# Optimization experiments

Measured on AMD Instinct MI355X. Metric: run time of the kernel, lower is better.

The kernel has to match this reference:

```python
import jax, jax.numpy as jnp
import numpy as np

N_QUBITS = 6
N_LAYERS = 2
QSVT_DEGREE = 3
DT_RANK = max(N_QUBITS // 2, 1)
OUT_DIM = 3 * N_QUBITS
PI = np.float32(np.pi)
DT_MIN, DT_MAX = 1e-3, 0.1
BATCH, SEQ = 256, 512


def _ry_mat(theta):
    c = jnp.cos(theta / 2)
    s = jnp.sin(theta / 2)
    row0 = jnp.stack([c, -s], axis=-1)
    row1 = jnp.stack([s, c], axis=-1)
    return jnp.stack([row0, row1], axis=-2).astype(jnp.complex64)


def _rz_mat(theta):
    e = jnp.exp(-0.5j * theta.astype(jnp.complex64))
    z = jnp.zeros_like(e)
    row0 = jnp.stack([e, z], axis=-1)
    row1 = jnp.stack([z, jnp.conj(e)], axis=-1)
    return jnp.stack([row0, row1], axis=-2)


def _rx_mat(theta):
    c = jnp.cos(theta / 2).astype(jnp.complex64)
    s = jnp.sin(theta / 2).astype(jnp.complex64)
    row0 = jnp.stack([c, -1j * s], axis=-1)
    row1 = jnp.stack([-1j * s, c], axis=-1)
    return jnp.stack([row0, row1], axis=-2)


def _apply1(state, mat, w):
    # state: (B, 2, ..., 2) tensor over N_QUBITS axes; mat: (2,2) or batched (B,2,2)
    state = jnp.moveaxis(state, 1 + w, -1)
    if mat.ndim == 3:
        state = jnp.einsum('bij,b...j->b...i', mat, state)
    else:
        state = jnp.einsum('ij,b...j->b...i', mat, state)
    return jnp.moveaxis(state, -1, 1 + w)


def _cnot(state, c, t):
    state = jnp.moveaxis(state, (1 + c, 1 + t), (-2, -1))
    state = state.at[..., 1, :].set(state[..., 1, ::-1])
    return jnp.moveaxis(state, (-2, -1), (1 + c, 1 + t))


def _crx(state, theta, c, t):
    state = jnp.moveaxis(state, (1 + c, 1 + t), (-2, -1))
    m = _rx_mat(theta)
    state = state.at[..., 1, :].set(jnp.einsum('ij,...j->...i', m, state[..., 1, :]))
    return jnp.moveaxis(state, (-2, -1), (1 + c, 1 + t))


def _circuit(h, x, dt, circuit_params, poly_coeffs, qsvt_params):
    """Batched statevector simulation of the selective QSVT + unified ansatz qnode."""
    n = N_QUBITS
    B = h.shape[0]
    state = jnp.zeros((B,) + (2,) * n, jnp.complex64)
    state = state.at[(slice(None),) + (0,) * n].set(1.0 + 0.0j)
    # 1) state encoding RY(h[t-1])
    for i in range(n):
        state = _apply1(state, _ry_mat(h[:, i]), i)
    # 2) Delta-modulated QSVT: RZ rotations + bidirectional CNOT ring per degree
    qidx = 0
    n_qp = n * QSVT_DEGREE
    for deg in range(QSVT_DEGREE + 1):
        coeff = poly_coeffs[deg]
        for i in range(n):
            if qidx < n_qp:
                ang = coeff * dt[:, i] * qsvt_params[qidx] * PI
                qidx += 1
            else:
                ang = coeff * dt[:, i] * PI
            state = _apply1(state, _rz_mat(ang), i)
        for i in range(n - 1):
            state = _cnot(state, i, i + 1)
        state = _cnot(state, n - 1, 0)
        for i in range(n - 1, 0, -1):
            state = _cnot(state, i, i - 1)
    # 3) unified variational ansatz
    p = 0
    for _ in range(N_LAYERS):
        for i in range(n):
            state = _apply1(state, _rx_mat(circuit_params[p]), i)
            state = _apply1(state, _ry_mat(circuit_params[p + 1]), i)
            state = _apply1(state, _rz_mat(circuit_params[p + 2]), i)
            p += 3
        for i in range(n):
            state = _crx(state, circuit_params[p], i, (i + 1) % n)
            p += 1
        for i in range(n - 1, -1, -1):
            state = _crx(state, circuit_params[p], i, (i - 1) % n)
            p += 1
    # 4) Delta-modulated input RY(x * dt)
    for i in range(n):
        state = _apply1(state, _ry_mat(x[:, i] * dt[:, i]), i)
    # 5) Pauli X/Y/Z expectation values per qubit
    xs, ys, zs = [], [], []
    for i in range(n):
        s = jnp.moveaxis(state, 1 + i, 1).reshape(B, 2, -1)
        z = jnp.sum(jnp.conj(s[:, 0]) * s[:, 1], axis=-1)
        xs.append(2.0 * jnp.real(z))
        ys.append(2.0 * jnp.imag(z))
        zs.append(jnp.sum(jnp.abs(s[:, 0]) ** 2 - jnp.abs(s[:, 1]) ** 2, axis=-1))
    return jnp.stack(xs + ys + zs, axis=-1).astype(jnp.float32)  # (B, 3n)


def setup_inputs() -> dict:
    key = jax.random.key(0)
    ks = jax.random.split(key, 8)
    angles = jax.random.uniform(ks[0], (BATCH, SEQ, N_QUBITS), jnp.float32) * PI
    Wx = jax.random.normal(ks[1], (DT_RANK + 2 * N_QUBITS, N_QUBITS), jnp.float32) / np.float32(np.sqrt(N_QUBITS))
    Wdt = jax.random.normal(ks[2], (N_QUBITS, DT_RANK), jnp.float32) / np.float32(np.sqrt(DT_RANK))
    dt = jnp.exp(jax.random.uniform(ks[3], (N_QUBITS,), jnp.float32) * np.float32(np.log(DT_MAX) - np.log(DT_MIN)) + np.float32(np.log(DT_MIN)))
    bdt = dt + jnp.log(-jnp.expm1(-dt))
    poly_coeffs = jax.random.normal(ks[4], (QSVT_DEGREE + 1,), jnp.float32) * 0.1
    qsvt_params = jax.random.normal(ks[5], (N_QUBITS * QSVT_DEGREE,), jnp.float32) * 0.1
    circuit_params = jax.random.normal(ks[6], (5 * N_QUBITS * N_LAYERS,), jnp.float32) * 0.1
    D = jnp.ones((OUT_DIM,), jnp.float32)
    Wc = jax.random.normal(ks[7], (OUT_DIM, N_QUBITS), jnp.float32) / np.float32(np.sqrt(N_QUBITS))
    return {"angles": angles, "Wx": Wx, "Wdt": Wdt, "bdt": bdt, "poly_coeffs": poly_coeffs, "qsvt_params": qsvt_params, "circuit_params": circuit_params, "D": D, "Wc": Wc}


def reference(angles, Wx, Wdt, bdt, poly_coeffs, qsvt_params, circuit_params, D, Wc):
    x_dbc = angles @ Wx.T  # (B,S, dt_rank + 2n)
    dt_raw = x_dbc[..., :DT_RANK]
    # B slice computed in the original but never used in forward
    C = x_dbc[..., DT_RANK + N_QUBITS:]
    dt_angles = jnp.tanh(jax.nn.softplus(dt_raw @ Wdt.T + bdt)) * PI  # (B,S,n)
    # quantum part is detached in the original (detach().cpu() before the qnode)
    sg = jax.lax.stop_gradient
    xs = (jnp.moveaxis(sg(angles), 1, 0), jnp.moveaxis(sg(dt_angles), 1, 0))
    cp, pc, qp = sg(circuit_params), sg(poly_coeffs), sg(qsvt_params)
    h0 = jnp.zeros((angles.shape[0], N_QUBITS), jnp.float32)

    def step(h, xt):
        x_t, dt_t = xt
        meas = _circuit(h, x_t, dt_t, cp, pc, qp)
        return meas[:, 2 * N_QUBITS:], meas  # carry = PauliZ block

    _, meas = jax.lax.scan(step, h0, xs)
    h_full = jnp.moveaxis(meas, 0, 1)  # (B,S,3n)
    return (C @ Wc.T) * h_full + D * jnp.concatenate([angles] * 3, axis=-1)
```

## Files before the change

### kernel.cpp

```cpp
#include <hip/hip_runtime.h>
#include <math.h>

#define BATCH 256
#define SEQ 512
#define SDS 54
#define PI_F 3.14159265358979323846f

template<int CTRL>
__device__ __forceinline__ float fdpp(float v) {
    return __int_as_float(__builtin_amdgcn_mov_dpp(__float_as_int(v), CTRL, 0xF, 0xF, true));
}
template<int L>
__device__ __forceinline__ float rdl(float v) {
    return __int_as_float(__builtin_amdgcn_readlane(__float_as_int(v), L));
}
__device__ __forceinline__ float rdlv(float v, int l) {
    return __int_as_float(__builtin_amdgcn_readlane(__float_as_int(v), l));
}
template<int M>
__device__ __forceinline__ float shxm(float v) {
    if constexpr (M == 1)       return fdpp<0xB1>(v);
    else if constexpr (M == 2)  return fdpp<0x4E>(v);
    else if constexpr (M == 8)  return fdpp<0x128>(v);
    else if constexpr (M == 32) return __shfl_xor(v, 32, 64);
    else return __int_as_float(__builtin_amdgcn_ds_swizzle(__float_as_int(v), (M << 10) | 0x1F));
}
__device__ __forceinline__ float redsum64(float v) {
    v += fdpp<0x128>(v);
    v += fdpp<0x124>(v);
    v += fdpp<0x122>(v);
    v += fdpp<0x121>(v);
    return (rdl<0>(v) + rdl<16>(v)) + (rdl<32>(v) + rdl<48>(v));
}
__device__ __forceinline__ float xorf(float v, int m) {
    return __int_as_float(__float_as_int(v) ^ m);
}
__device__ __forceinline__ void wg_barrier_lds() {
    __builtin_amdgcn_sched_barrier(0);
    __builtin_amdgcn_s_waitcnt(0xC07F);
    __builtin_amdgcn_s_barrier();
    __builtin_amdgcn_sched_barrier(0);
}
__device__ __forceinline__ int permf(int x) {
    const int cs[11] = {0,1,2,3,4,5,5,4,3,2,1};
    const int ts[11] = {1,2,3,4,5,0,4,3,2,1,0};
#pragma unroll
    for (int k = 10; k >= 0; k--) {
        int cb = (x >> (5 - cs[k])) & 1;
        x ^= cb << (5 - ts[k]);
    }
    return x;
}
__device__ __forceinline__ void cmul4(const float* c,
    float vr, float vi, float ar, float ai, float br, float bi, float cr, float ci,
    float& nr, float& ni) {
    nr = c[0]*vr - c[1]*vi + c[2]*ar - c[3]*ai + c[4]*br - c[5]*bi + c[6]*cr - c[7]*ci;
    ni = c[0]*vi + c[1]*vr + c[2]*ai + c[3]*ar + c[4]*bi + c[5]*br + c[6]*ci + c[7]*cr;
}
__device__ __forceinline__ void ringapply(const float* rc,
    float vr, float vi, float br, float bi, float cr, float ci, float dr, float di,
    float& nr, float& ni) {
    nr = rc[0]*vr - rc[1]*bi - rc[2]*ci + rc[3]*dr;
    ni = rc[0]*vi + rc[1]*br + rc[2]*cr + rc[3]*di;
}

__global__ __launch_bounds__(256) void prep_kernel(
    const float* __restrict__ angles, const float* __restrict__ Wx,
    const float* __restrict__ Wdt, const float* __restrict__ bdt,
    const float* __restrict__ D, const float* __restrict__ Wc,
    float* __restrict__ sd)
{
    int gid = blockIdx.x * blockDim.x + threadIdx.x;
    if (gid >= BATCH * SEQ) return;
    const float* a = angles + (size_t)gid * 6;
    float ang[6];
#pragma unroll
    for (int i = 0; i < 6; i++) ang[i] = a[i];
    float dtr[3];
#pragma unroll
    for (int r = 0; r < 3; r++) {
        float s = 0.f;
#pragma unroll
        for (int k = 0; k < 6; k++) s += ang[k] * Wx[r * 6 + k];
        dtr[r] = s;
    }
    float* rec = sd + (size_t)gid * SDS;
    float dtv[6];
#pragma unroll
    for (int i = 0; i < 6; i++) {
        float x = bdt[i];
#pragma unroll
        for (int r = 0; r < 3; r++) x += dtr[r] * Wdt[i * 3 + r];
        float sp = (x > 15.f) ? x : log1pf(expf(x));
        dtv[i] = tanhf(sp) * PI_F;
        rec[i] = dtv[i];
        float th = ang[i] * dtv[i];
        rec[6 + i]  = 0.5f * cosf(th);
        rec[12 + i] = 0.5f * sinf(th);
    }
    float C[6];
#pragma unroll
    for (int i = 0; i < 6; i++) {
        float s = 0.f;
#pragma unroll
        for (int k = 0; k < 6; k++) s += ang[k] * Wx[(9 + i) * 6 + k];
        C[i] = s;
    }
#pragma unroll
    for (int j = 0; j < 18; j++) {
        float s = 0.f;
#pragma unroll
        for (int i = 0; i < 6; i++) s += C[i] * Wc[j * 6 + i];
        rec[18 + j] = (j < 6 || j >= 12) ? 2.f * s : s;
        rec[36 + j] = D[j] * ang[j % 6];
    }
}

__global__ __launch_bounds__(64) void umat_kernel(const float* __restrict__ cp,
                                                  float2* __restrict__ um)
{
    const int lane = threadIdx.x;
    const int col = blockIdx.x;
    int bitv[6];
#pragma unroll
    for (int i = 0; i < 6; i++) bitv[i] = (lane >> (5 - i)) & 1;

    float qc[2][3][8], rc[2][6][4];
#pragma unroll
    for (int l = 0; l < 2; l++) {
        float g00r[6], g00i[6], g01r[6], g01i[6], g10r[6], g10i[6], g11r[6], g11i[6];
#pragma unroll
        for (int i = 0; i < 6; i++) {
            float ax = cp[l * 30 + i * 3 + 0];
            float ay = cp[l * 30 + i * 3 + 1];
            float az = cp[l * 30 + i * 3 + 2];
            float ca = cosf(0.5f * ax), sa = sinf(0.5f * ax);
            float cb = cosf(0.5f * ay), sb = sinf(0.5f * ay);
            float cg = cosf(0.5f * az), sg = sinf(0.5f * az);
            float m00r = cb * ca, m00i =  sb * sa;
            float m01r = -sb * ca, m01i = -cb * sa;
            float m10r =  sb * ca, m10i = -cb * sa;
            float m11r =  cb * ca, m11i = -sb * sa;
            g00r[i] = cg * m00r + sg * m00i; g00i[i] = cg * m00i - sg * m00r;
            g01r[i] = cg * m01r + sg * m01i; g01i[i] = cg * m01i - sg * m01r;
            g10r[i] = cg * m10r - sg * m10i; g10i[i] = cg * m10i + sg * m10r;
            g11r[i] = cg * m11r - sg * m11i; g11i[i] = cg * m11i + sg * m11r;
        }
#pragma unroll
        for (int pp = 0; pp < 3; pp++) {
            int aq = 2 * pp, bq = 2 * pp + 1;
            float dar = bitv[aq] ? g11r[aq] : g00r[aq], dai = bitv[aq] ? g11i[aq] : g00i[aq];
            float oar = bitv[aq] ? g10r[aq] : g01r[aq], oai = bitv[aq] ? g10i[aq] : g01i[aq];
            float dbr = bitv[bq] ? g11r[bq] : g00r[bq], dbi = bitv[bq] ? g11i[bq] : g00i[bq];
            float obr = bitv[bq] ? g10r[bq] : g01r[bq], obi = bitv[bq] ? g10i[bq] : g01i[bq];
            qc[l][pp][0] = dar * dbr - dai * dbi;  qc[l][pp][1] = dar * dbi + dai * dbr;
            qc[l][pp][2] = oar * dbr - oai * dbi;  qc[l][pp][3] = oar * dbi + oai * dbr;
            qc[l][pp][4] = dar * obr - dai * obi;  qc[l][pp][5] = dar * obi + dai * obr;
            qc[l][pp][6] = oar * obr - oai * obi;  qc[l][pp][7] = oar * obi + oai * obr;
        }
        const int Aq[6] = {0, 2, 4, 5, 3, 1};
        const int Bq[6] = {1, 3, 5, 4, 2, 0};
#pragma unroll
        for (int o = 0; o < 6; o++) {
            float tha = (o < 3) ? cp[l * 30 + 18 + 2 * o]     : cp[l * 30 + 24 + 2 * (o - 3)];
            float thb = (o < 3) ? cp[l * 30 + 18 + 2 * o + 1] : cp[l * 30 + 24 + 2 * (o - 3) + 1];
            float ca = cosf(0.5f * tha), sa = sinf(0.5f * tha);
            float cb = cosf(0.5f * thb), sb = sinf(0.5f * thb);
            int ba = bitv[Aq[o]], bb = bitv[Bq[o]];
            float mx0 = ba ? ca : 1.f, sae = ba ? sa : 0.f;
            float ny0 = bb ? cb : 1.f, sbe = bb ? sb : 0.f;
            rc[l][o][0] = ny0 * mx0; rc[l][o][1] = -ny0 * sae;
            rc[l][o][2] = -mx0 * sbe; rc[l][o][3] = -sae * sbe;
        }
    }

    float re = (lane == col) ? 1.f : 0.f;
    float im = 0.f;
    auto p1q = [&](int mi, int mj, const float* c) {
        float ar = __shfl_xor(re, mi, 64), ai = __shfl_xor(im, mi, 64);
        float br = __shfl_xor(re, mj, 64), bi = __shfl_xor(im, mj, 64);
        float cr = __shfl_xor(re, mi | mj, 64), ci = __shfl_xor(im, mi | mj, 64);
        float nr, ni;
        cmul4(c, re, im, ar, ai, br, bi, cr, ci, nr, ni);
        re = nr; im = ni;
    };
    auto rng = [&](int mb, int mc, const float* c) {
        float br = __shfl_xor(re, mb, 64), bi = __shfl_xor(im, mb, 64);
        float cr = __shfl_xor(re, mc, 64), ci = __shfl_xor(im, mc, 64);
        float dr = __shfl_xor(re, mb | mc, 64), di = __shfl_xor(im, mb | mc, 64);
        float nr, ni;
        ringapply(c, re, im, br, bi, cr, ci, dr, di, nr, ni);
        re = nr; im = ni;
    };
#pragma unroll
    for (int l = 0; l < 2; l++) {
        p1q(32, 16, qc[l][0]);
        p1q(8, 4, qc[l][1]);
        p1q(2, 1, qc[l][2]);
        rng(16, 8, rc[l][0]);
        rng(4, 2, rc[l][1]);
        rng(1, 32, rc[l][2]);
        rng(2, 4, rc[l][3]);
        rng(8, 16, rc[l][4]);
        rng(32, 1, rc[l][5]);
    }
    um[(size_t)lane * 64 + col] = make_float2(re, im);
}

__global__ __launch_bounds__(256, 1) void step_kernel(
    const float* __restrict__ sd, const float* __restrict__ pc,
    const float* __restrict__ qp, const float2* __restrict__ um,
    float* __restrict__ out)
{
    __shared__ float2 sPart[2][4][64];
    const int tid = threadIdx.x;
    const int wave = tid >> 6;
    const int lane = tid & 63;
    const int b = blockIdx.x;

    int bitv[6];
#pragma unroll
    for (int i = 0; i < 6; i++) bitv[i] = (lane >> (5 - i)) & 1;
    int sflip[6];
    float sgnf[6];
#pragma unroll
    for (int q = 0; q < 6; q++) {
        sflip[q] = bitv[q] ? (int)0x80000000 : 0;
        sgnf[q]  = bitv[q] ? -1.f : 1.f;
    }

    const int jbase = wave * 16;
    float2 row[16];
#pragma unroll
    for (int jj = 0; jj < 16; jj++) row[jj] = um[(size_t)lane * 64 + jbase + jj];

    float A[6], sel[6];
    {
        int x1 = permf(lane), x2 = permf(x1), x3 = permf(x2), x4 = permf(x3);
#pragma unroll
        for (int i = 0; i < 6; i++) {
            float u0 = pc[0] * PI_F * qp[0 * 6 + i];
            float u1 = pc[1] * PI_F * qp[1 * 6 + i];
            float u2 = pc[2] * PI_F * qp[2 * 6 + i];
            float u3 = pc[3] * PI_F;
            float t1 = ((x1 >> (5 - i)) & 1) ? 0.5f : -0.5f;
            float t2 = ((x2 >> (5 - i)) & 1) ? 0.5f : -0.5f;
            float t3 = ((x3 >> (5 - i)) & 1) ? 0.5f : -0.5f;
            float t4 = ((x4 >> (5 - i)) & 1) ? 0.5f : -0.5f;
            A[i] = u3 * t1 + u2 * t2 + u1 * t3 + u0 * t4;
            sel[i] = (float)((x4 >> (5 - i)) & 1);
        }
    }

    auto b6 = [&](float v) -> float {
        float g;
        g = shxm<1>(v);  v = fmaf(sgnf[5], v, g);
        g = shxm<2>(v);  v = fmaf(sgnf[4], v, g);
        g = shxm<4>(v);  v = fmaf(sgnf[3], v, g);
        g = shxm<8>(v);  v = fmaf(sgnf[2], v, g);
        g = shxm<16>(v); v = fmaf(sgnf[1], v, g);
        g = shxm<32>(v); v = fmaf(sgnf[0], v, g);
        return v;
    };
    auto b6c = [&](float& vr, float& vi) {
#define BSTG(M, SI) { float gr = shxm<M>(vr), gi = shxm<M>(vi); \
                      vr = fmaf(sgnf[SI], vr, gr); vi = fmaf(sgnf[SI], vi, gi); }
        BSTG(1, 5) BSTG(2, 4) BSTG(4, 3) BSTG(8, 2) BSTG(16, 1) BSTG(32, 0)
#undef BSTG
    };

    const float* sdb = sd + (size_t)b * SEQ * SDS;
    float* outb = out + (size_t)b * SEQ * 18;

    float hh0 = 0.f, hh1 = 0.f, hh2 = 0.f, hh3 = 0.f, hh4 = 0.f, hh5 = 0.f;

    float bufA[18], bufB[18];
    {
        const float2* p2 = (const float2*)sdb;
#pragma unroll
        for (int k = 0; k < 9; k++) {
            float2 v = p2[k];
            bufA[2 * k] = v.x; bufA[2 * k + 1] = v.y;
        }
    }

    auto body = [&](float (&cur)[18], float (&nxt)[18], int t, int pp) {
        {
            int tn = (t + 1 < SEQ) ? t + 1 : t;
            const float2* rn2 = (const float2*)(sdb + (size_t)tn * SDS);
#pragma unroll
            for (int k = 0; k < 9; k++) {
                float2 v = rn2[k];
                nxt[2 * k] = v.x; nxt[2 * k + 1] = v.y;
            }
        }

        float phi = A[0]*cur[0] + A[1]*cur[1] + A[2]*cur[2]
                  + A[3]*cur[3] + A[4]*cur[4] + A[5]*cur[5];
        float sph, cph;
        __sincosf(phi, &sph, &cph);

        float ss0, cc0, ss1, cc1, ss2, cc2, ss3, cc3, ss4, cc4, ss5, cc5;
        __sincosf(hh0, &ss0, &cc0);
        __sincosf(hh1, &ss1, &cc1);
        __sincosf(hh2, &ss2, &cc2);
        __sincosf(hh3, &ss3, &cc3);
        __sincosf(hh4, &ss4, &cc4);
        __sincosf(hh5, &ss5, &cc5);
        float f0 = fmaf(sel[0], ss0 - cc0, cc0);
        float f1 = fmaf(sel[1], ss1 - cc1, cc1);
        float f2 = fmaf(sel[2], ss2 - cc2, cc2);
        float f3 = fmaf(sel[3], ss3 - cc3, cc3);
        float f4 = fmaf(sel[4], ss4 - cc4, cc4);
        float f5 = fmaf(sel[5], ss5 - cc5, cc5);
        float prod = ((f0 * f1) * (f2 * f3)) * (f4 * f5);
        float pr = prod * cph, pi = prod * sph;

        float ar0 = 0.f, ai0 = 0.f, ar1 = 0.f, ai1 = 0.f;
#pragma unroll
        for (int jj = 0; jj < 16; jj += 2) {
            float sr0 = rdlv(pr, jbase + jj);
            float si0 = rdlv(pi, jbase + jj);
            float sr1 = rdlv(pr, jbase + jj + 1);
            float si1 = rdlv(pi, jbase + jj + 1);
            ar0 = fmaf(row[jj].x, sr0, ar0);
            ar0 = fmaf(-row[jj].y, si0, ar0);
            ai0 = fmaf(row[jj].x, si0, ai0);
            ai0 = fmaf(row[jj].y, sr0, ai0);
            ar1 = fmaf(row[jj + 1].x, sr1, ar1);
            ar1 = fmaf(-row[jj + 1].y, si1, ar1);
            ai1 = fmaf(row[jj + 1].x, si1, ai1);
            ai1 = fmaf(row[jj + 1].y, sr1, ai1);
        }
        sPart[pp][wave][lane] = make_float2(ar0 + ar1, ai0 + ai1);
        wg_barrier_lds();
        float2 q0v = sPart[pp][0][lane], q1v = sPart[pp][1][lane];
        float2 q2v = sPart[pp][2][lane], q3v = sPart[pp][3][lane];
        float re = (q0v.x + q1v.x) + (q2v.x + q3v.x);
        float im = (q0v.y + q1v.y) + (q2v.y + q3v.y);

        float P  = fmaf(re, re, im * im);
        float Wp = b6(P);
        float Rr = re, Ri = im;
        b6c(Rr, Ri);
        float Q  = fmaf(Rr, Rr, Ri * Ri) * 0.015625f;
        float Wq = b6(Q);

        float Z0 = rdl<32>(Wp), Z1 = rdl<16>(Wp), Z2 = rdl<8>(Wp);
        float Z3 = rdl<4>(Wp),  Z4 = rdl<2>(Wp),  Z5 = rdl<1>(Wp);
        float X0 = rdl<32>(Wq), X1 = rdl<16>(Wq), X2 = rdl<8>(Wq);
        float X3 = rdl<4>(Wq),  X4 = rdl<2>(Wq),  X5 = rdl<1>(Wq);

        hh0 = cur[6]  * Z0 - cur[12] * X0;
        hh1 = cur[7]  * Z1 - cur[13] * X1;
        hh2 = cur[8]  * Z2 - cur[14] * X2;
        hh3 = cur[9]  * Z3 - cur[15] * X3;
        hh4 = cur[10] * Z4 - cur[16] * X4;
        hh5 = cur[11] * Z5 - cur[17] * X5;

        float* o = outb + (size_t)t * 18;
        if (wave == 0) {
            if (lane == 0) {
                float2* o2 = (float2*)o;
                o2[0] = make_float2(Z0, Z1); o2[1] = make_float2(Z2, Z3);
                o2[2] = make_float2(Z4, Z5); o2[3] = make_float2(X0, X1);
                o2[4] = make_float2(X2, X3); o2[5] = make_float2(X4, X5);
            }
        } else if (wave == 1) {
            float Gr = shxm<32>(Rr), Gi = shxm<32>(Ri);
            float u0 = xorf(fmaf(-Ri, Gr, Rr * Gi), sflip[0]);
            Gr = shxm<16>(Rr); Gi = shxm<16>(Ri);
            float u1 = xorf(fmaf(-Ri, Gr, Rr * Gi), sflip[1]);
            float Y0 = redsum64(u0) * -0.015625f;
            float Y1 = redsum64(u1) * -0.015625f;
            if (lane == 0) ((float2*)(o + 12))[0] = make_float2(Y0, Y1);
        } else if (wave == 2) {
            float Gr = shxm<8>(Rr), Gi = shxm<8>(Ri);
            float u0 = xorf(fmaf(-Ri, Gr, Rr * Gi), sflip[2]);
            Gr = shxm<4>(Rr); Gi = shxm<4>(Ri);
            float u1 = xorf(fmaf(-Ri, Gr, Rr * Gi), sflip[3]);
            float Y2 = redsum64(u0) * -0.015625f;
            float Y3 = redsum64(u1) * -0.015625f;
            if (lane == 0) ((float2*)(o + 14))[0] = make_float2(Y2, Y3);
        } else {
            float Gr = shxm<2>(Rr), Gi = shxm<2>(Ri);
            float u0 = xorf(fmaf(-Ri, Gr, Rr * Gi), sflip[4]);
            Gr = shxm<1>(Rr); Gi = shxm<1>(Ri);
            float u1 = xorf(fmaf(-Ri, Gr, Rr * Gi), sflip[5]);
            float Y4 = redsum64(u0) * -0.015625f;
            float Y5 = redsum64(u1) * -0.015625f;
            if (lane == 0) ((float2*)(o + 16))[0] = make_float2(Y4, Y5);
        }
    };

    for (int t = 0; t < SEQ; t += 2) {
        body(bufA, bufB, t, 0);
        body(bufB, bufA, t + 1, 1);
    }
}

__global__ __launch_bounds__(256) void post_kernel(
    const float* __restrict__ sd, float* __restrict__ out)
{
    int gid = blockIdx.x * blockDim.x + threadIdx.x;
    if (gid >= BATCH * SEQ) return;
    const float* rec = sd + (size_t)gid * SDS;
    float* o = out + (size_t)gid * 18;

    float zxy[18];
    {
        const float2* o2 = (const float2*)o;
#pragma unroll
        for (int k = 0; k < 9; k++) {
            float2 v = o2[k];
            zxy[2 * k] = v.x; zxy[2 * k + 1] = v.y;
        }
    }
    float r[54];
    {
        const float2* r2 = (const float2*)rec;
#pragma unroll
        for (int k = 3; k < 27; k++) {
            float2 v = r2[k];
            r[2 * k] = v.x; r[2 * k + 1] = v.y;
        }
    }
    float res[18];
#pragma unroll
    for (int q = 0; q < 6; q++) {
        float Z = zxy[q], X = zxy[6 + q], Y = zxy[12 + q];
        float c = r[6 + q], s = r[12 + q];
        float px = c * X + s * Z;
        float hq = c * Z - s * X;
        res[q]      = fmaf(r[18 + q], px, r[36 + q]);
        res[6 + q]  = fmaf(r[24 + q], Y,  r[42 + q]);
        res[12 + q] = fmaf(r[30 + q], hq, r[48 + q]);
    }
    float2* ow = (float2*)o;
#pragma unroll
    for (int k = 0; k < 9; k++) ow[k] = make_float2(res[2 * k], res[2 * k + 1]);
}

extern "C" void kernel_launch(void* const* d_in, const int* in_sizes, int n_in,
                              void* d_out, int out_size, void* d_ws, size_t ws_size,
                              hipStream_t stream) {
    const float* angles = (const float*)d_in[0];
    const float* Wx     = (const float*)d_in[1];
    const float* Wdt    = (const float*)d_in[2];
    const float* bdt    = (const float*)d_in[3];
    const float* pc     = (const float*)d_in[4];
    const float* qp     = (const float*)d_in[5];
    const float* cp     = (const float*)d_in[6];
    const float* D      = (const float*)d_in[7];
    const float* Wc     = (const float*)d_in[8];
    float* sd  = (float*)d_ws;
    float2* um = (float2*)(sd + (size_t)BATCH * SEQ * SDS);
    float* out = (float*)d_out;

    umat_kernel<<<64, 64, 0, stream>>>(cp, um);
    prep_kernel<<<(BATCH * SEQ) / 256, 256, 0, stream>>>(angles, Wx, Wdt, bdt, D, Wc, sd);
    step_kernel<<<BATCH, 256, 0, stream>>>(sd, pc, qp, um, out);
    post_kernel<<<(BATCH * SEQ) / 256, 256, 0, stream>>>(sd, out);
}
```

Baseline: 720.9 us.

## Collapse step kernel to one wave per batch with LDS-broadcast matvec

```diff
diff --git a/kernel.cpp b/kernel.cpp
--- a/kernel.cpp
+++ b/kernel.cpp
@@ -13,9 +13,6 @@
 template<int L>
 __device__ __forceinline__ float rdl(float v) {
     return __int_as_float(__builtin_amdgcn_readlane(__float_as_int(v), L));
-}
-__device__ __forceinline__ float rdlv(float v, int l) {
-    return __int_as_float(__builtin_amdgcn_readlane(__float_as_int(v), l));
 }
 template<int M>
 __device__ __forceinline__ float shxm(float v) {
@@ -35,10 +32,9 @@
 __device__ __forceinline__ float xorf(float v, int m) {
     return __int_as_float(__float_as_int(v) ^ m);
 }
-__device__ __forceinline__ void wg_barrier_lds() {
+__device__ __forceinline__ void wave_lds_sync() {
     __builtin_amdgcn_sched_barrier(0);
     __builtin_amdgcn_s_waitcnt(0xC07F);
-    __builtin_amdgcn_s_barrier();
     __builtin_amdgcn_sched_barrier(0);
 }
 __device__ __forceinline__ int permf(int x) {
@@ -207,15 +203,19 @@
     um[(size_t)lane * 64 + col] = make_float2(re, im);
 }
 
-__global__ __launch_bounds__(256, 1) void step_kernel(
-    const float* __restrict__ sd, const float* __restrict__ pc,
+#define CMAC(AR, AI, UU, PRv, PIv)           \
+    AR = fmaf((UU).x, (PRv), AR);            \
+    AR = fmaf(-(UU).y, (PIv), AR);           \
+    AI = fmaf((UU).x, (PIv), AI);            \
+    AI = fmaf((UU).y, (PRv), AI);
+
+__global__ __launch_bounds__(64, 1) void step_kernel(
+    const float* __restrict__ sd, const float* __restrict__ pcf,
     const float* __restrict__ qp, const float2* __restrict__ um,
     float* __restrict__ out)
 {
-    __shared__ float2 sPart[2][4][64];
-    const int tid = threadIdx.x;
-    const int wave = tid >> 6;
-    const int lane = tid & 63;
+    __shared__ __align__(16) float2 sP[64];
+    const int lane = threadIdx.x;
     const int b = blockIdx.x;
 
     int bitv[6];
@@ -229,20 +229,19 @@
         sgnf[q]  = bitv[q] ? -1.f : 1.f;
     }
 
-    const int jbase = wave * 16;
-    float2 row[16];
-#pragma unroll
-    for (int jj = 0; jj < 16; jj++) row[jj] = um[(size_t)lane * 64 + jbase + jj];
+    float2 row[64];
+#pragma unroll
+    for (int c = 0; c < 64; c++) row[c] = um[(size_t)lane * 64 + c];
 
     float A[6], sel[6];
     {
         int x1 = permf(lane), x2 = permf(x1), x3 = permf(x2), x4 = permf(x3);
 #pragma unroll
         for (int i = 0; i < 6; i++) {
-            float u0 = pc[0] * PI_F * qp[0 * 6 + i];
-            float u1 = pc[1] * PI_F * qp[1 * 6 + i];
-            float u2 = pc[2] * PI_F * qp[2 * 6 + i];
-            float u3 = pc[3] * PI_F;
+            float u0 = pcf[0] * PI_F * qp[0 * 6 + i];
+            float u1 = pcf[1] * PI_F * qp[1 * 6 + i];
+            float u2 = pcf[2] * PI_F * qp[2 * 6 + i];
+            float u3 = pcf[3] * PI_F;
             float t1 = ((x1 >> (5 - i)) & 1) ? 0.5f : -0.5f;
             float t2 = ((x2 >> (5 - i)) & 1) ? 0.5f : -0.5f;
             float t3 = ((x3 >> (5 - i)) & 1) ? 0.5f : -0.5f;
@@ -284,7 +283,7 @@
         }
     }
 
-    auto body = [&](float (&cur)[18], float (&nxt)[18], int t, int pp) {
+    auto body = [&](float (&cur)[18], float (&nxt)[18], int t) {
         {
             int tn = (t + 1 < SEQ) ? t + 1 : t;
             const float2* rn2 = (const float2*)(sdb + (size_t)tn * SDS);
@@ -316,28 +315,28 @@
         float prod = ((f0 * f1) * (f2 * f3)) * (f4 * f5);
         float pr = prod * cph, pi = prod * sph;
 
-        float ar0 = 0.f, ai0 = 0.f, ar1 = 0.f, ai1 = 0.f;
-#pragma unroll
-        for (int jj = 0; jj < 16; jj += 2) {
-            float sr0 = rdlv(pr, jbase + jj);
-            float si0 = rdlv(pi, jbase + jj);
-            float sr1 = rdlv(pr, jbase + jj + 1);
-            float si1 = rdlv(pi, jbase + jj + 1);
-            ar0 = fmaf(row[jj].x, sr0, ar0);
-            ar0 = fmaf(-row[jj].y, si0, ar0);
-            ai0 = fmaf(row[jj].x, si0, ai0);
-            ai0 = fmaf(row[jj].y, sr0, ai0);
-            ar1 = fmaf(row[jj + 1].x, sr1, ar1);
-            ar1 = fmaf(-row[jj + 1].y, si1, ar1);
-            ai1 = fmaf(row[jj + 1].x, si1, ai1);
-            ai1 = fmaf(row[jj + 1].y, sr1, ai1);
-        }
-        sPart[pp][wave][lane] = make_float2(ar0 + ar1, ai0 + ai1);
-        wg_barrier_lds();
-        float2 q0v = sPart[pp][0][lane], q1v = sPart[pp][1][lane];
-        float2 q2v = sPart[pp][2][lane], q3v = sPart[pp][3][lane];
-        float re = (q0v.x + q1v.x) + (q2v.x + q3v.x);
-        float im = (q0v.y + q1v.y) + (q2v.y + q3v.y);
+        sP[lane] = make_float2(pr, pi);
+        wave_lds_sync();
+
+        float a0r = 0.f, a0i = 0.f, a1r = 0.f, a1i = 0.f;
+        float a2r = 0.f, a2i = 0.f, a3r = 0.f, a3i = 0.f;
+#pragma unroll
+        for (int c = 0; c < 64; c += 8) {
+            float4 q0 = *reinterpret_cast<const float4*>(&sP[c + 0]);
+            float4 q1 = *reinterpret_cast<const float4*>(&sP[c + 2]);
+            float4 q2 = *reinterpret_cast<const float4*>(&sP[c + 4]);
+            float4 q3 = *reinterpret_cast<const float4*>(&sP[c + 6]);
+            CMAC(a0r, a0i, row[c + 0], q0.x, q0.y)
+            CMAC(a1r, a1i, row[c + 1], q0.z, q0.w)
+            CMAC(a2r, a2i, row[c + 2], q1.x, q1.y)
+            CMAC(a3r, a3i, row[c + 3], q1.z, q1.w)
+            CMAC(a0r, a0i, row[c + 4], q2.x, q2.y)
+            CMAC(a1r, a1i, row[c + 5], q2.z, q2.w)
+            CMAC(a2r, a2i, row[c + 6], q3.x, q3.y)
+            CMAC(a3r, a3i, row[c + 7], q3.z, q3.w)
+        }
+        float re = (a0r + a1r) + (a2r + a3r);
+        float im = (a0i + a1i) + (a2i + a3i);
 
         float P  = fmaf(re, re, im * im);
         float Wp = b6(P);
@@ -358,46 +357,40 @@
         hh4 = cur[10] * Z4 - cur[16] * X4;
         hh5 = cur[11] * Z5 - cur[17] * X5;
 
-        float* o = outb + (size_t)t * 18;
-        if (wave == 0) {
-            if (lane == 0) {
-                float2* o2 = (float2*)o;
-                o2[0] = make_float2(Z0, Z1); o2[1] = make_float2(Z2, Z3);
-                o2[2] = make_float2(Z4, Z5); o2[3] = make_float2(X0, X1);
-                o2[4] = make_float2(X2, X3); o2[5] = make_float2(X4, X5);
-            }
-        } else if (wave == 1) {
-            float Gr = shxm<32>(Rr), Gi = shxm<32>(Ri);
-            float u0 = xorf(fmaf(-Ri, Gr, Rr * Gi), sflip[0]);
-            Gr = shxm<16>(Rr); Gi = shxm<16>(Ri);
-            float u1 = xorf(fmaf(-Ri, Gr, Rr * Gi), sflip[1]);
-            float Y0 = redsum64(u0) * -0.015625f;
-            float Y1 = redsum64(u1) * -0.015625f;
-            if (lane == 0) ((float2*)(o + 12))[0] = make_float2(Y0, Y1);
-        } else if (wave == 2) {
-            float Gr = shxm<8>(Rr), Gi = shxm<8>(Ri);
-            float u0 = xorf(fmaf(-Ri, Gr, Rr * Gi), sflip[2]);
-            Gr = shxm<4>(Rr); Gi = shxm<4>(Ri);
-            float u1 = xorf(fmaf(-Ri, Gr, Rr * Gi), sflip[3]);
-            float Y2 = redsum64(u0) * -0.015625f;
-            float Y3 = redsum64(u1) * -0.015625f;
-            if (lane == 0) ((float2*)(o + 14))[0] = make_float2(Y2, Y3);
-        } else {
-            float Gr = shxm<2>(Rr), Gi = shxm<2>(Ri);
-            float u0 = xorf(fmaf(-Ri, Gr, Rr * Gi), sflip[4]);
-            Gr = shxm<1>(Rr); Gi = shxm<1>(Ri);
-            float u1 = xorf(fmaf(-Ri, Gr, Rr * Gi), sflip[5]);
-            float Y4 = redsum64(u0) * -0.015625f;
-            float Y5 = redsum64(u1) * -0.015625f;
-            if (lane == 0) ((float2*)(o + 16))[0] = make_float2(Y4, Y5);
+        float Yv[6];
+        {
+            float gr, gi;
+            gr = shxm<32>(re); gi = shxm<32>(im);
+            Yv[0] = redsum64(xorf(fmaf(re, gi, -(im * gr)), sflip[0]));
+            gr = shxm<16>(re); gi = shxm<16>(im);
+            Yv[1] = redsum64(xorf(fmaf(re, gi, -(im * gr)), sflip[1]));
+            gr = shxm<8>(re);  gi = shxm<8>(im);
+            Yv[2] = redsum64(xorf(fmaf(re, gi, -(im * gr)), sflip[2]));
+            gr = shxm<4>(re);  gi = shxm<4>(im);
+            Yv[3] = redsum64(xorf(fmaf(re, gi, -(im * gr)), sflip[3]));
+            gr = shxm<2>(re);  gi = shxm<2>(im);
+            Yv[4] = redsum64(xorf(fmaf(re, gi, -(im * gr)), sflip[4]));
+            gr = shxm<1>(re);  gi = shxm<1>(im);
+            Yv[5] = redsum64(xorf(fmaf(re, gi, -(im * gr)), sflip[5]));
+        }
+
+        if (lane == 0) {
+            float2* o2 = (float2*)(outb + (size_t)t * 18);
+            o2[0] = make_float2(Z0, Z1); o2[1] = make_float2(Z2, Z3);
+            o2[2] = make_float2(Z4, Z5); o2[3] = make_float2(X0, X1);
+            o2[4] = make_float2(X2, X3); o2[5] = make_float2(X4, X5);
+            o2[6] = make_float2(Yv[0], Yv[1]);
+            o2[7] = make_float2(Yv[2], Yv[3]);
+            o2[8] = make_float2(Yv[4], Yv[5]);
         }
     };
 
     for (int t = 0; t < SEQ; t += 2) {
-        body(bufA, bufB, t, 0);
-        body(bufB, bufA, t + 1, 1);
-    }
-}
+        body(bufA, bufB, t);
+        body(bufB, bufA, t + 1);
+    }
+}
+#undef CMAC
 
 __global__ __launch_bounds__(256) void post_kernel(
     const float* __restrict__ sd, float* __restrict__ out)
@@ -459,6 +452,6 @@
 
     umat_kernel<<<64, 64, 0, stream>>>(cp, um);
     prep_kernel<<<(BATCH * SEQ) / 256, 256, 0, stream>>>(angles, Wx, Wdt, bdt, D, Wc, sd);
-    step_kernel<<<BATCH, 256, 0, stream>>>(sd, pc, qp, um, out);
+    step_kernel<<<BATCH, 64, 0, stream>>>(sd, pc, qp, um, out);
     post_kernel<<<(BATCH * SEQ) / 256, 256, 0, stream>>>(sd, out);
 }
```

Measured after the change: 963.9 us. +33.7%, slower.

## Compute X/Y expectations directly via lane-pair products and pipeline phase sincos

Applied to the files above, without the earlier changes.

```diff
diff --git a/kernel.cpp b/kernel.cpp
--- a/kernel.cpp
+++ b/kernel.cpp
@@ -5,6 +5,7 @@
 #define SEQ 512
 #define SDS 54
 #define PI_F 3.14159265358979323846f
+#define INV2PI_F 0.15915494309189535f
 
 template<int CTRL>
 __device__ __forceinline__ float fdpp(float v) {
@@ -17,20 +18,38 @@
 __device__ __forceinline__ float rdlv(float v, int l) {
     return __int_as_float(__builtin_amdgcn_readlane(__float_as_int(v), l));
 }
-template<int M>
-__device__ __forceinline__ float shxm(float v) {
-    if constexpr (M == 1)       return fdpp<0xB1>(v);
-    else if constexpr (M == 2)  return fdpp<0x4E>(v);
-    else if constexpr (M == 8)  return fdpp<0x128>(v);
-    else if constexpr (M == 32) return __shfl_xor(v, 32, 64);
-    else return __int_as_float(__builtin_amdgcn_ds_swizzle(__float_as_int(v), (M << 10) | 0x1F));
-}
+__device__ __forceinline__ float x1f(float v) { return fdpp<0xB1>(v); }
+__device__ __forceinline__ float x2f(float v) { return fdpp<0x4E>(v); }
+__device__ __forceinline__ float x4f(float v) { return fdpp<0x141>(fdpp<0x1B>(v)); }
+__device__ __forceinline__ float x8f(float v) { return fdpp<0x128>(v); }
+#if __has_builtin(__builtin_amdgcn_permlane16_swap)
+__device__ __forceinline__ float sum16(float v) {
+    typedef unsigned int u2v __attribute__((ext_vector_type(2)));
+    u2v r = __builtin_amdgcn_permlane16_swap(__float_as_uint(v), __float_as_uint(v), false, false);
+    return __uint_as_float(r[0]) + __uint_as_float(r[1]);
+}
+#else
+__device__ __forceinline__ float sum16(float v) {
+    return v + __int_as_float(__builtin_amdgcn_ds_swizzle(__float_as_int(v), (16 << 10) | 0x1F));
+}
+#endif
+#if __has_builtin(__builtin_amdgcn_permlane32_swap)
+__device__ __forceinline__ float sum32(float v) {
+    typedef unsigned int u2v __attribute__((ext_vector_type(2)));
+    u2v r = __builtin_amdgcn_permlane32_swap(__float_as_uint(v), __float_as_uint(v), false, false);
+    return __uint_as_float(r[0]) + __uint_as_float(r[1]);
+}
+#else
+__device__ __forceinline__ float sum32(float v) { return v + __shfl_xor(v, 32, 64); }
+#endif
 __device__ __forceinline__ float redsum64(float v) {
     v += fdpp<0x128>(v);
     v += fdpp<0x124>(v);
     v += fdpp<0x122>(v);
     v += fdpp<0x121>(v);
-    return (rdl<0>(v) + rdl<16>(v)) + (rdl<32>(v) + rdl<48>(v));
+    v = sum16(v);
+    v = sum32(v);
+    return v;
 }
 __device__ __forceinline__ float xorf(float v, int m) {
     return __int_as_float(__float_as_int(v) ^ m);
@@ -207,8 +226,14 @@
     um[(size_t)lane * 64 + col] = make_float2(re, im);
 }
 
+#define CMACR(AR, AI, UU, SR, SI)            \
+    AR = fmaf((UU).x, (SR), AR);             \
+    AR = fmaf(-(UU).y, (SI), AR);            \
+    AI = fmaf((UU).x, (SI), AI);             \
+    AI = fmaf((UU).y, (SR), AI);
+
 __global__ __launch_bounds__(256, 1) void step_kernel(
-    const float* __restrict__ sd, const float* __restrict__ pc,
+    const float* __restrict__ sd, const float* __restrict__ pcf,
     const float* __restrict__ qp, const float2* __restrict__ um,
     float* __restrict__ out)
 {
@@ -228,6 +253,8 @@
         sflip[q] = bitv[q] ? (int)0x80000000 : 0;
         sgnf[q]  = bitv[q] ? -1.f : 1.f;
     }
+    const float w0 = bitv[0] ? -2.f : 0.f;
+    const float w1 = bitv[1] ? -2.f : 0.f;
 
     const int jbase = wave * 16;
     float2 row[16];
@@ -239,10 +266,10 @@
         int x1 = permf(lane), x2 = permf(x1), x3 = permf(x2), x4 = permf(x3);
 #pragma unroll
         for (int i = 0; i < 6; i++) {
-            float u0 = pc[0] * PI_F * qp[0 * 6 + i];
-            float u1 = pc[1] * PI_F * qp[1 * 6 + i];
-            float u2 = pc[2] * PI_F * qp[2 * 6 + i];
-            float u3 = pc[3] * PI_F;
+            float u0 = pcf[0] * PI_F * qp[0 * 6 + i];
+            float u1 = pcf[1] * PI_F * qp[1 * 6 + i];
+            float u2 = pcf[2] * PI_F * qp[2 * 6 + i];
+            float u3 = pcf[3] * PI_F;
             float t1 = ((x1 >> (5 - i)) & 1) ? 0.5f : -0.5f;
             float t2 = ((x2 >> (5 - i)) & 1) ? 0.5f : -0.5f;
             float t3 = ((x3 >> (5 - i)) & 1) ? 0.5f : -0.5f;
@@ -254,59 +281,52 @@
 
     auto b6 = [&](float v) -> float {
         float g;
-        g = shxm<1>(v);  v = fmaf(sgnf[5], v, g);
-        g = shxm<2>(v);  v = fmaf(sgnf[4], v, g);
-        g = shxm<4>(v);  v = fmaf(sgnf[3], v, g);
-        g = shxm<8>(v);  v = fmaf(sgnf[2], v, g);
-        g = shxm<16>(v); v = fmaf(sgnf[1], v, g);
-        g = shxm<32>(v); v = fmaf(sgnf[0], v, g);
+        g = x1f(v); v = fmaf(sgnf[5], v, g);
+        g = x2f(v); v = fmaf(sgnf[4], v, g);
+        g = x4f(v); v = fmaf(sgnf[3], v, g);
+        g = x8f(v); v = fmaf(sgnf[2], v, g);
+        v = fmaf(w1, v, sum16(v));
+        v = fmaf(w0, v, sum32(v));
         return v;
     };
-    auto b6c = [&](float& vr, float& vi) {
-#define BSTG(M, SI) { float gr = shxm<M>(vr), gi = shxm<M>(vi); \
-                      vr = fmaf(sgnf[SI], vr, gr); vi = fmaf(sgnf[SI], vi, gi); }
-        BSTG(1, 5) BSTG(2, 4) BSTG(4, 3) BSTG(8, 2) BSTG(16, 1) BSTG(32, 0)
-#undef BSTG
-    };
 
     const float* sdb = sd + (size_t)b * SEQ * SDS;
     float* outb = out + (size_t)b * SEQ * 18;
 
     float hh0 = 0.f, hh1 = 0.f, hh2 = 0.f, hh3 = 0.f, hh4 = 0.f, hh5 = 0.f;
 
-    float bufA[18], bufB[18];
-    {
-        const float2* p2 = (const float2*)sdb;
+    float buf0[18], buf1[18], buf2[18];
+    auto ldrec = [&](float (&dst)[18], int t) {
+        const float2* p2 = (const float2*)(sdb + (size_t)t * SDS);
 #pragma unroll
         for (int k = 0; k < 9; k++) {
             float2 v = p2[k];
-            bufA[2 * k] = v.x; bufA[2 * k + 1] = v.y;
-        }
-    }
-
-    auto body = [&](float (&cur)[18], float (&nxt)[18], int t, int pp) {
-        {
-            int tn = (t + 1 < SEQ) ? t + 1 : t;
-            const float2* rn2 = (const float2*)(sdb + (size_t)tn * SDS);
-#pragma unroll
-            for (int k = 0; k < 9; k++) {
-                float2 v = rn2[k];
-                nxt[2 * k] = v.x; nxt[2 * k + 1] = v.y;
-            }
-        }
-
-        float phi = A[0]*cur[0] + A[1]*cur[1] + A[2]*cur[2]
-                  + A[3]*cur[3] + A[4]*cur[4] + A[5]*cur[5];
-        float sph, cph;
-        __sincosf(phi, &sph, &cph);
-
-        float ss0, cc0, ss1, cc1, ss2, cc2, ss3, cc3, ss4, cc4, ss5, cc5;
-        __sincosf(hh0, &ss0, &cc0);
-        __sincosf(hh1, &ss1, &cc1);
-        __sincosf(hh2, &ss2, &cc2);
-        __sincosf(hh3, &ss3, &cc3);
-        __sincosf(hh4, &ss4, &cc4);
-        __sincosf(hh5, &ss5, &cc5);
+            dst[2 * k] = v.x; dst[2 * k + 1] = v.y;
+        }
+    };
+    ldrec(buf0, 0);
+    ldrec(buf1, 1);
+
+    float sphC, cphC;
+    {
+        float phi = A[0]*buf0[0] + A[1]*buf0[1] + A[2]*buf0[2]
+                  + A[3]*buf0[3] + A[4]*buf0[4] + A[5]*buf0[5];
+        float u = phi * INV2PI_F;
+        u = u - floorf(u);
+        sphC = __builtin_amdgcn_sinf(u);
+        cphC = __builtin_amdgcn_cosf(u);
+    }
+
+    auto body = [&](float (&cur)[18], float (&nxt)[18], float (&far)[18], int t) {
+        const int pp = t & 1;
+        ldrec(far, (t + 2 < SEQ) ? t + 2 : SEQ - 1);
+
+        float ss0 = __builtin_amdgcn_sinf(hh0 * INV2PI_F), cc0 = __builtin_amdgcn_cosf(hh0 * INV2PI_F);
+        float ss1 = __builtin_amdgcn_sinf(hh1 * INV2PI_F), cc1 = __builtin_amdgcn_cosf(hh1 * INV2PI_F);
+        float ss2 = __builtin_amdgcn_sinf(hh2 * INV2PI_F), cc2 = __builtin_amdgcn_cosf(hh2 * INV2PI_F);
+        float ss3 = __builtin_amdgcn_sinf(hh3 * INV2PI_F), cc3 = __builtin_amdgcn_cosf(hh3 * INV2PI_F);
+        float ss4 = __builtin_amdgcn_sinf(hh4 * INV2PI_F), cc4 = __builtin_amdgcn_cosf(hh4 * INV2PI_F);
+        float ss5 = __builtin_amdgcn_sinf(hh5 * INV2PI_F), cc5 = __builtin_amdgcn_cosf(hh5 * INV2PI_F);
         float f0 = fmaf(sel[0], ss0 - cc0, cc0);
         float f1 = fmaf(sel[1], ss1 - cc1, cc1);
         float f2 = fmaf(sel[2], ss2 - cc2, cc2);
@@ -314,7 +334,16 @@
         float f4 = fmaf(sel[4], ss4 - cc4, cc4);
         float f5 = fmaf(sel[5], ss5 - cc5, cc5);
         float prod = ((f0 * f1) * (f2 * f3)) * (f4 * f5);
-        float pr = prod * cph, pi = prod * sph;
+        float pr = prod * cphC, pi = prod * sphC;
+
+        {
+            float phi = A[0]*nxt[0] + A[1]*nxt[1] + A[2]*nxt[2]
+                      + A[3]*nxt[3] + A[4]*nxt[4] + A[5]*nxt[5];
+            float u = phi * INV2PI_F;
+            u = u - floorf(u);
+            sphC = __builtin_amdgcn_sinf(u);
+            cphC = __builtin_amdgcn_cosf(u);
+        }
 
         float ar0 = 0.f, ai0 = 0.f, ar1 = 0.f, ai1 = 0.f;
 #pragma unroll
@@ -323,14 +352,8 @@
             float si0 = rdlv(pi, jbase + jj);
             float sr1 = rdlv(pr, jbase + jj + 1);
             float si1 = rdlv(pi, jbase + jj + 1);
-            ar0 = fmaf(row[jj].x, sr0, ar0);
-            ar0 = fmaf(-row[jj].y, si0, ar0);
-            ai0 = fmaf(row[jj].x, si0, ai0);
-            ai0 = fmaf(row[jj].y, sr0, ai0);
-            ar1 = fmaf(row[jj + 1].x, sr1, ar1);
-            ar1 = fmaf(-row[jj + 1].y, si1, ar1);
-            ai1 = fmaf(row[jj + 1].x, si1, ai1);
-            ai1 = fmaf(row[jj + 1].y, sr1, ai1);
+            CMACR(ar0, ai0, row[jj], sr0, si0)
+            CMACR(ar1, ai1, row[jj + 1], sr1, si1)
         }
         sPart[pp][wave][lane] = make_float2(ar0 + ar1, ai0 + ai1);
         wg_barrier_lds();
@@ -341,15 +364,22 @@
 
         float P  = fmaf(re, re, im * im);
         float Wp = b6(P);
-        float Rr = re, Ri = im;
-        b6c(Rr, Ri);
-        float Q  = fmaf(Rr, Rr, Ri * Ri) * 0.015625f;
-        float Wq = b6(Q);
-
         float Z0 = rdl<32>(Wp), Z1 = rdl<16>(Wp), Z2 = rdl<8>(Wp);
         float Z3 = rdl<4>(Wp),  Z4 = rdl<2>(Wp),  Z5 = rdl<1>(Wp);
-        float X0 = rdl<32>(Wq), X1 = rdl<16>(Wq), X2 = rdl<8>(Wq);
-        float X3 = rdl<4>(Wq),  X4 = rdl<2>(Wq),  X5 = rdl<1>(Wq);
+
+        float g32r = sum32(re) - re, g32i = sum32(im) - im;
+        float g16r = sum16(re) - re, g16i = sum16(im) - im;
+        float g8r  = x8f(re),        g8i  = x8f(im);
+        float g4r  = x4f(re),        g4i  = x4f(im);
+        float g2r  = x2f(re),        g2i  = x2f(im);
+        float g1r  = x1f(re),        g1i  = x1f(im);
+
+        float X0 = redsum64(fmaf(re, g32r, im * g32i));
+        float X1 = redsum64(fmaf(re, g16r, im * g16i));
+        float X2 = redsum64(fmaf(re, g8r,  im * g8i));
+        float X3 = redsum64(fmaf(re, g4r,  im * g4i));
+        float X4 = redsum64(fmaf(re, g2r,  im * g2i));
+        float X5 = redsum64(fmaf(re, g1r,  im * g1i));
 
         hh0 = cur[6]  * Z0 - cur[12] * X0;
         hh1 = cur[7]  * Z1 - cur[13] * X1;
@@ -367,37 +397,29 @@
                 o2[4] = make_float2(X2, X3); o2[5] = make_float2(X4, X5);
             }
         } else if (wave == 1) {
-            float Gr = shxm<32>(Rr), Gi = shxm<32>(Ri);
-            float u0 = xorf(fmaf(-Ri, Gr, Rr * Gi), sflip[0]);
-            Gr = shxm<16>(Rr); Gi = shxm<16>(Ri);
-            float u1 = xorf(fmaf(-Ri, Gr, Rr * Gi), sflip[1]);
-            float Y0 = redsum64(u0) * -0.015625f;
-            float Y1 = redsum64(u1) * -0.015625f;
+            float Y0 = redsum64(xorf(fmaf(re, g32i, -(im * g32r)), sflip[0]));
+            float Y1 = redsum64(xorf(fmaf(re, g16i, -(im * g16r)), sflip[1]));
             if (lane == 0) ((float2*)(o + 12))[0] = make_float2(Y0, Y1);
         } else if (wave == 2) {
-            float Gr = shxm<8>(Rr), Gi = shxm<8>(Ri);
-            float u0 = xorf(fmaf(-Ri, Gr, Rr * Gi), sflip[2]);
-            Gr = shxm<4>(Rr); Gi = shxm<4>(Ri);
-            float u1 = xorf(fmaf(-Ri, Gr, Rr * Gi), sflip[3]);
-            float Y2 = redsum64(u0) * -0.015625f;
-            float Y3 = redsum64(u1) * -0.015625f;
+            float Y2 = redsum64(xorf(fmaf(re, g8i, -(im * g8r)), sflip[2]));
+            float Y3 = redsum64(xorf(fmaf(re, g4i, -(im * g4r)), sflip[3]));
             if (lane == 0) ((float2*)(o + 14))[0] = make_float2(Y2, Y3);
         } else {
-            float Gr = shxm<2>(Rr), Gi = shxm<2>(Ri);
-            float u0 = xorf(fmaf(-Ri, Gr, Rr * Gi), sflip[4]);
-            Gr = shxm<1>(Rr); Gi = shxm<1>(Ri);
-            float u1 = xorf(fmaf(-Ri, Gr, Rr * Gi), sflip[5]);
-            float Y4 = redsum64(u0) * -0.015625f;
-            float Y5 = redsum64(u1) * -0.015625f;
+            float Y4 = redsum64(xorf(fmaf(re, g2i, -(im * g2r)), sflip[4]));
+            float Y5 = redsum64(xorf(fmaf(re, g1i, -(im * g1r)), sflip[5]));
             if (lane == 0) ((float2*)(o + 16))[0] = make_float2(Y4, Y5);
         }
     };
 
-    for (int t = 0; t < SEQ; t += 2) {
-        body(bufA, bufB, t, 0);
-        body(bufB, bufA, t + 1, 1);
-    }
-}
+    for (int t = 0; t < 510; t += 3) {
+        body(buf0, buf1, buf2, t);
+        body(buf1, buf2, buf0, t + 1);
+        body(buf2, buf0, buf1, t + 2);
+    }
+    body(buf0, buf1, buf2, 510);
+    body(buf1, buf2, buf0, 511);
+}
+#undef CMACR
 
 __global__ __launch_bounds__(256) void post_kernel(
     const float* __restrict__ sd, float* __restrict__ out)
```

Result: no change. 708.3 us (-1.8%).
